# Optimization experiments

Measured on AMD Instinct MI355X. Metric: run time of the kernel, lower is better.

## Reference

```python
import jax, jax.numpy as jnp
import numpy as np

BN_EPS = 1e-3


def _bn(x, gamma, beta):
    # training-mode BatchNorm1d: per-call batch statistics (biased variance)
    m = jnp.mean(x, axis=0)
    v = jnp.mean(jnp.square(x - m), axis=0)
    return gamma * (x - m) * jax.lax.rsqrt(v + BN_EPS) + beta


def setup_inputs() -> dict:
    key = jax.random.key(0)
    ks = jax.random.split(key, 8)
    N, V, Cin, Cout = 1_000_000, 100_000, 16, 64
    return {
        "feat": jax.random.normal(ks[0], (V, Cin), dtype=jnp.float32),
        "points_xyz": jax.random.normal(ks[1], (N, Cin), dtype=jnp.float32),
        "unq_inv": jax.random.randint(ks[2], (N,), 0, V),
        "W_pre": jax.random.normal(ks[3], (Cin, Cout), dtype=jnp.float32) * (1.0 / np.sqrt(Cin)),
        "b_pre": jnp.zeros((Cout,), dtype=jnp.float32),
        "gamma_pre": jnp.ones((Cout,), dtype=jnp.float32),
        "beta_pre": jnp.zeros((Cout,), dtype=jnp.float32),
        "W_pos": jax.random.normal(ks[4], (Cout, Cout), dtype=jnp.float32) * (1.0 / np.sqrt(Cout)),
        "b_pos": jnp.zeros((Cout,), dtype=jnp.float32),
        "gamma_n": jnp.ones((Cout,), dtype=jnp.float32),
        "beta_n": jnp.zeros((Cout,), dtype=jnp.float32),
    }


def reference(feat, points_xyz, unq_inv, W_pre, b_pre, gamma_pre, beta_pre,
              W_pos, b_pos, gamma_n, beta_n):
    V = feat.shape[0]
    # per-point branch: pre_mix (Linear + BN), sin/cos gating, scatter-add to voxels
    p = _bn(points_xyz @ W_pre + b_pre, gamma_pre, beta_pre)      # [N, Cout]
    pw = p @ W_pos + b_pos                                        # [N, Cout]
    feat_add_sin = jax.ops.segment_sum(p * jnp.sin(pw), unq_inv, num_segments=V)  # [V, Cout]
    feat_add_cos = jax.ops.segment_sum(p * jnp.cos(pw), unq_inv, num_segments=V)
    # per-voxel (center) branch through the SAME pre_mix / pos_weight layers
    f = _bn(feat @ W_pre + b_pre, gamma_pre, beta_pre)            # [V, Cout]
    mw = f @ W_pos + b_pos
    center_sin = f * jnp.sin(mw)
    center_cos = f * jnp.cos(mw)
    final = (feat_add_sin + center_sin) * center_sin + (feat_add_cos + center_cos) * center_cos
    return jax.nn.relu(_bn(final, gamma_n, beta_n))
```

## Files before the change

kernel.cpp:

```cpp
#include <hip/hip_runtime.h>
#include <cstdint>
#include <cstddef>

constexpr int CIN  = 16;
constexpr int COUT = 64;
constexpr int NMOM = 16 + 136;
constexpr double BN_EPS = 1e-3;

typedef float v2f __attribute__((ext_vector_type(2)));
typedef __fp16 v2h __attribute__((ext_vector_type(2)));
constexpr float INV_2PI = 0.15915494309189535f;

constexpr int P_A = 0, P_B = 64, P_C = 128, P_WC = 192, P_SZ = 192 + CIN * COUT;

constexpr int CHUNK = 512;
constexpr int MB = 256;

__device__ __forceinline__ unsigned bc_u(v2h h) { return __builtin_bit_cast(unsigned, h); }
__device__ __forceinline__ v2h bc_h(unsigned u) { return __builtin_bit_cast(v2h, u); }

__global__ __launch_bounds__(256, 2) void moments2_kernel(const float* __restrict__ xyz, int n1,
                                                       const float* __restrict__ feat, int n2,
                                                       const int* __restrict__ unq,
                                                       int* __restrict__ cnt,
                                                       float* __restrict__ partP,
                                                       float* __restrict__ partF)
{
    const int bb  = blockIdx.x;
    const bool second = (bb >= MB);
    const float* x = second ? feat : xyz;
    const int    n = second ? n2 : n1;
    float* part    = second ? partF : partP;
    const int blk  = second ? bb - MB : bb;

    float acc[NMOM];
#pragma unroll
    for (int i = 0; i < NMOM; i++) acc[i] = 0.f;

    int tid = blk * 256 + threadIdx.x;
    int stride = MB * 256;
    for (int r = tid; r < n; r += stride) {
        const float4* xp = (const float4*)(x + (size_t)r * CIN);
        float4 a0 = xp[0], a1 = xp[1], a2 = xp[2], a3 = xp[3];
        if (!second) atomicAdd(cnt + unq[r], 1);
        float v[16] = {a0.x,a0.y,a0.z,a0.w, a1.x,a1.y,a1.z,a1.w,
                       a2.x,a2.y,a2.z,a2.w, a3.x,a3.y,a3.z,a3.w};
#pragma unroll
        for (int i = 0; i < 16; i++) acc[i] += v[i];
        int c = 16;
#pragma unroll
        for (int k = 0; k < 16; k++)
#pragma unroll
            for (int l = k; l < 16; l++) { acc[c] = fmaf(v[k], v[l], acc[c]); c++; }
    }

    const int lane = threadIdx.x & 63;
    const int wid  = threadIdx.x >> 6;
    float r0 = 0.f, r1 = 0.f, r2 = 0.f;
#pragma unroll
    for (int i = 0; i < NMOM; i++) {
        float s = acc[i];
#pragma unroll
        for (int off = 1; off < 64; off <<= 1) s += __shfl_xor(s, off, 64);
        if (i < 64)       { if (lane == i)       r0 = s; }
        else if (i < 128) { if (lane == i - 64)  r1 = s; }
        else              { if (lane == i - 128) r2 = s; }
    }

    __shared__ float red[4][NMOM];
    red[wid][lane] = r0;
    red[wid][64 + lane] = r1;
    if (lane < NMOM - 128) red[wid][128 + lane] = r2;
    __syncthreads();
    int t = threadIdx.x;
    if (t < NMOM) {
        float s = red[0][t] + red[1][t] + red[2][t] + red[3][t];
        part[(size_t)blk * NMOM + t] = s;
    }
}

__global__ __launch_bounds__(256) void prep_kernel(const float* __restrict__ Wpre, const float* __restrict__ bpre,
                            const float* __restrict__ gpre, const float* __restrict__ bepre,
                            const float* __restrict__ Wpos, const float* __restrict__ bpos,
                            const float* __restrict__ partP, const float* __restrict__ partF,
                            int nrows, int Np, int Vv,
                            float* __restrict__ prepP, float* __restrict__ prepF)
{
    const int t  = threadIdx.x;
    const int br = blockIdx.x;
    const float* part = br ? partF : partP;
    const double n    = br ? (double)Vv : (double)Np;
    const double inv_n = 1.0 / n;
    float* prep       = br ? prepF : prepP;

    __shared__ float sWpre[CIN * 64];
    __shared__ float sWpos[64 * 64];
    __shared__ double mom[NMOM];
    __shared__ double sS[64], sB[64];

    for (int i = t; i < CIN * 64; i += 256) sWpre[i] = Wpre[i];
    for (int i = t; i < 64 * 64; i += 256)  sWpos[i] = Wpos[i];

    if (t < NMOM) {
        double s0 = 0, s1 = 0, s2 = 0, s3 = 0, s4 = 0, s5 = 0, s6 = 0, s7 = 0;
        int r = 0;
        for (; r + 8 <= nrows; r += 8) {
            s0 += (double)part[(size_t)(r + 0) * NMOM + t];
            s1 += (double)part[(size_t)(r + 1) * NMOM + t];
            s2 += (double)part[(size_t)(r + 2) * NMOM + t];
            s3 += (double)part[(size_t)(r + 3) * NMOM + t];
            s4 += (double)part[(size_t)(r + 4) * NMOM + t];
            s5 += (double)part[(size_t)(r + 5) * NMOM + t];
            s6 += (double)part[(size_t)(r + 6) * NMOM + t];
            s7 += (double)part[(size_t)(r + 7) * NMOM + t];
        }
        for (; r < nrows; r++) s0 += (double)part[(size_t)r * NMOM + t];
        mom[t] = ((s0 + s1) + (s2 + s3)) + ((s4 + s5) + (s6 + s7));
    }
    __syncthreads();

    if (t < 64) {
        const int k = t;
        double mu[16];
#pragma unroll
        for (int i = 0; i < 16; i++) mu[i] = mom[i] * inv_n;
        double w[16];
#pragma unroll
        for (int i = 0; i < 16; i++) w[i] = (double)sWpre[i * 64 + k];

        double mk = (double)bpre[k];
#pragma unroll
        for (int i = 0; i < 16; i++) mk += mu[i] * w[i];

        double var = 0.0;
        int c = 16;
#pragma unroll
        for (int a = 0; a < 16; a++)
#pragma unroll
            for (int l = a; l < 16; l++) {
                double cov = mom[c] * inv_n - mu[a] * mu[l]; c++;
                var += (a == l ? 1.0 : 2.0) * w[a] * w[l] * cov;
            }

        double s_k = (double)gpre[k] / sqrt(var + BN_EPS);
        double B_k = (double)bepre[k] + s_k * ((double)bpre[k] - mk);
        sS[k] = s_k; sB[k] = B_k;
    }
    __syncthreads();

    if (t < 64) {
        const int k = t;
        double c0 = (double)bpos[k], c1 = 0.0;
        for (int j = 0; j < 64; j += 2) {
            c0 += sB[j]     * (double)sWpos[j * 64 + k];
            c1 += sB[j + 1] * (double)sWpos[(j + 1) * 64 + k];
        }
        prep[P_A + k] = (float)sS[k];
        prep[P_B + k] = (float)sB[k];
        prep[P_C + k] = (float)(c0 + c1);
    }

    {
        const int k  = t & 63;
        const int i0 = t >> 6;
        for (int i = i0; i < 16; i += 4) {
            double w0 = 0.0, w1 = 0.0;
            for (int j = 0; j < 64; j += 2) {
                w0 += (double)sWpre[i * 64 + j]     * sS[j]     * (double)sWpos[j * 64 + k];
                w1 += (double)sWpre[i * 64 + j + 1] * sS[j + 1] * (double)sWpos[(j + 1) * 64 + k];
            }
            prep[P_WC + i * 64 + k] = (float)(w0 + w1);
        }
    }
}

__global__ __launch_bounds__(256) void scan_a(const int* __restrict__ cnt, int V,
                                              int* __restrict__ chunkSum)
{
    const int b = blockIdx.x, t = threadIdx.x;
    int base = b * CHUNK;
    int i0 = base + t * 2, i1 = i0 + 1;
    int s = ((i0 < V) ? cnt[i0] : 0) + ((i1 < V) ? cnt[i1] : 0);
    __shared__ int red[4];
    const int lane = t & 63, wid = t >> 6;
#pragma unroll
    for (int off = 1; off < 64; off <<= 1) s += __shfl_xor(s, off, 64);
    if (lane == 0) red[wid] = s;
    __syncthreads();
    if (t == 0) chunkSum[b] = red[0] + red[1] + red[2] + red[3];
}

__global__ __launch_bounds__(256) void scan_b(const int* __restrict__ chunkSum, int nch,
                                              int* __restrict__ chunkBase,
                                              int* __restrict__ start, int V, int N)
{
    const int t = threadIdx.x;
    __shared__ int a[256];
    int v = (t < nch) ? chunkSum[t] : 0;
    a[t] = v;
    __syncthreads();
    for (int off = 1; off < 256; off <<= 1) {
        int add = (t >= off) ? a[t - off] : 0;
        __syncthreads();
        a[t] += add;
        __syncthreads();
    }
    chunkBase[t] = a[t] - v;
    if (t == 0) start[V] = N;
}

__global__ __launch_bounds__(64) void scan_c(const int* __restrict__ cnt, int V,
                                             const int* __restrict__ chunkBase,
                                             int* __restrict__ start)
{
    const int b = blockIdx.x;
    const int lane = threadIdx.x;
    const int base = b * CHUNK + lane * 8;
    int e[8];
    int run = 0;
#pragma unroll
    for (int j = 0; j < 8; j++) {
        int idx = base + j;
        int c = (idx < V) ? cnt[idx] : 0;
        e[j] = run;
        run += c;
    }
    int incl = run;
#pragma unroll
    for (int off = 1; off < 64; off <<= 1) {
        int vv = __shfl_up(incl, off, 64);
        if (lane >= off) incl += vv;
    }
    int excl = incl - run;
    int myBase = chunkBase[b] + excl;
#pragma unroll
    for (int j = 0; j < 8; j++) {
        int idx = base + j;
        if (idx < V) start[idx] = myBase + e[j];
    }
}

__global__ __launch_bounds__(256) void scatter_kernel(const int* __restrict__ unq, int N,
                                                      const int* __restrict__ start,
                                                      int* __restrict__ cursor,
                                                      int* __restrict__ sortedIdx)
{
    int t = blockIdx.x * blockDim.x + threadIdx.x;
    int stride = gridDim.x * blockDim.x;
    for (; t < N; t += stride) {
        int v = unq[t];
        int pos = start[v] + atomicAdd(cursor + v, 1);
        sortedIdx[pos] = t;
    }
}

__global__ __launch_bounds__(256) void fused_pass(const float* __restrict__ xyz,
                                                  const float* __restrict__ feat,
                                                  const int* __restrict__ sortedIdx,
                                                  const int* __restrict__ start,
                                                  const float* __restrict__ Wpre,
                                                  const float* __restrict__ prepP,
                                                  const float* __restrict__ prepF,
                                                  float* __restrict__ outFinal,
                                                  float* __restrict__ statsPart, int V)
{
    const int lane = threadIdx.x & 63;
    const int wid  = threadIdx.x >> 6;
    const int rq   = lane >> 2;
    const int cc   = lane & 3;

    __shared__ uint2 ldsq[4][3][64];
    __shared__ unsigned sWcF2[8 * 64];
    uint2* bufA = ldsq[wid][0];
    uint2* bufB = ldsq[wid][1];
    uint2* remb = ldsq[wid][2];
    const int wslot = rq * 4 + cc;

    for (int i = threadIdx.x; i < 8 * 64; i += 256) {
        int fi = i >> 6, ch = i & 63;
        sWcF2[i] = bc_u(__builtin_amdgcn_cvt_pkrtz(prepF[P_WC + (2 * fi) * 64 + ch],
                                                   prepF[P_WC + (2 * fi + 1) * 64 + ch]));
    }
    __syncthreads();

    v2h wpre2[8], wcp2[8];
#pragma unroll
    for (int i = 0; i < 8; i++) {
        wpre2[i] = __builtin_amdgcn_cvt_pkrtz(Wpre[(2 * i) * 64 + lane],
                                              Wpre[(2 * i + 1) * 64 + lane]);
        wcp2[i]  = __builtin_amdgcn_cvt_pkrtz(prepP[P_WC + (2 * i) * 64 + lane],
                                              prepP[P_WC + (2 * i + 1) * 64 + lane]);
    }

    const float AP = prepP[P_A + lane], BP = prepP[P_B + lane];
    const float CPr = prepP[P_C + lane] * INV_2PI;
    const float AF = prepF[P_A + lane], BF = prepF[P_B + lane];
    const float CFr = prepF[P_C + lane] * INV_2PI;

    const int wave = __builtin_amdgcn_readfirstlane((int)((blockIdx.x * blockDim.x + threadIdx.x) >> 6));
    const int nw   = (gridDim.x * blockDim.x) >> 6;
    float s1 = 0.f, s2 = 0.f;

    auto prefetch = [&](int v, int& sb, int& m, uint2& u) {
        sb = __builtin_amdgcn_readfirstlane(start[v]);
        int se = __builtin_amdgcn_readfirstlane(start[v + 1]);
        m = se - sb;
        int ms0 = min(m, 15);
        int row = min(rq, ms0);
        int ridx = sortedIdx[sb + row];
        const float* bp = (row == ms0) ? (feat + (size_t)v * CIN)
                                       : (xyz  + (size_t)ridx * CIN);
        float4 q = *(const float4*)(bp + cc * 4);
        u.x = bc_u(__builtin_amdgcn_cvt_pkrtz(q.x, q.y));
        u.y = bc_u(__builtin_amdgcn_cvt_pkrtz(q.z, q.w));
    };

    auto pointmath = [&](const uint2* buf, int j, v2f& acc) {
        uint4 a = ((const uint4*)buf)[j * 2 + 0];
        uint4 b = ((const uint4*)buf)[j * 2 + 1];
        v2h xs[8] = {bc_h(a.x), bc_h(a.y), bc_h(a.z), bc_h(a.w),
                     bc_h(b.x), bc_h(b.y), bc_h(b.z), bc_h(b.w)};
        float dx = 0.f, dw = 0.f;
#pragma unroll
        for (int i = 0; i < 8; i++) {
            dx = __builtin_amdgcn_fdot2(xs[i], wpre2[i], dx, false);
            dw = __builtin_amdgcn_fdot2(xs[i], wcp2[i],  dw, false);
        }
        float p  = fmaf(AP, dx, BP);
        float r  = fmaf(dw, INV_2PI, CPr);
        float sv = __builtin_amdgcn_sinf(r);
        float cv = __builtin_amdgcn_cosf(r);
        acc += p * (v2f){sv, cv};
    };

    int v = wave;
    int sb = 0, m = 0;
    uint2* cur = bufA;
    uint2* nxt = bufB;
    if (v < V) {
        uint2 u; prefetch(v, sb, m, u);
        cur[wslot] = u;
    }

    while (v < V) {
        const int vn = v + nw;
        int sbn = 0, mn = 0; uint2 un = {};
        if (vn < V) prefetch(vn, sbn, mn, un);

        const int ms0 = min(m, 15);
        v2f acc = (v2f){0.f, 0.f};

        for (int j = 0; j < ms0; j++) pointmath(cur, j, acc);

        for (int base = 15; base < m; base += 16) {
            const int msr  = min(16, m - base);
            const int rowc = min(rq, msr - 1);
            int ridx = sortedIdx[sb + base + rowc];
            float4 q = *(const float4*)(xyz + (size_t)ridx * CIN + cc * 4);
            uint2 u;
            u.x = bc_u(__builtin_amdgcn_cvt_pkrtz(q.x, q.y));
            u.y = bc_u(__builtin_amdgcn_cvt_pkrtz(q.z, q.w));
            remb[wslot] = u;
            for (int j = 0; j < msr; j++) pointmath(remb, j, acc);
        }

        {
            uint4 a = ((const uint4*)cur)[ms0 * 2 + 0];
            uint4 b = ((const uint4*)cur)[ms0 * 2 + 1];
            v2h xs[8] = {bc_h(a.x), bc_h(a.y), bc_h(a.z), bc_h(a.w),
                         bc_h(b.x), bc_h(b.y), bc_h(b.z), bc_h(b.w)};
            float dx = 0.f, dw = 0.f;
#pragma unroll
            for (int i = 0; i < 8; i++) {
                dx = __builtin_amdgcn_fdot2(xs[i], wpre2[i], dx, false);
                dw = __builtin_amdgcn_fdot2(xs[i], bc_h(sWcF2[i * 64 + lane]), dw, false);
            }
            float f  = fmaf(AF, dx, BF);
            float r  = fmaf(dw, INV_2PI, CFr);
            float sv = __builtin_amdgcn_sinf(r);
            float cv = __builtin_amdgcn_cosf(r);
            float cs = f * sv, ccn = f * cv;
            float fin = fmaf(acc.x + cs, cs, (acc.y + ccn) * ccn);
            outFinal[(size_t)v * 64 + lane] = fin;
            s1 += fin;
            s2 = fmaf(fin, fin, s2);
        }

        if (vn < V) nxt[wslot] = un;
        uint2* tmp = cur; cur = nxt; nxt = tmp;
        v = vn; sb = sbn; m = mn;
    }

    __shared__ float sh1[4][64], sh2[4][64];
    sh1[wid][lane] = s1; sh2[wid][lane] = s2;
    __syncthreads();
    if (threadIdx.x < 64) {
        float t1 = sh1[0][lane] + sh1[1][lane] + sh1[2][lane] + sh1[3][lane];
        float t2 = sh2[0][lane] + sh2[1][lane] + sh2[2][lane] + sh2[3][lane];
        float* row = statsPart + (size_t)(blockIdx.x & 63) * 128;
        atomicAdd(row + lane, t1);
        atomicAdd(row + 64 + lane, t2);
    }
}

__global__ __launch_bounds__(256) void norm_kernel(float* __restrict__ out,
                                                   const float* __restrict__ sp,
                                                   const float* __restrict__ gn,
                                                   const float* __restrict__ bnb,
                                                   int V, size_t n4)
{
    __shared__ float sNs[64], sNb[64];
    const int t = threadIdx.x;
    if (t < 64) {
        double u1 = 0.0, u2 = 0.0;
#pragma unroll 4
        for (int r = 0; r < 64; r++) {
            u1 += (double)sp[(size_t)r * 128 + t];
            u2 += (double)sp[(size_t)r * 128 + 64 + t];
        }
        double mean = u1 / (double)V;
        double var  = u2 / (double)V - mean * mean;
        double ns   = (double)gn[t] / sqrt(var + BN_EPS);
        sNs[t] = (float)ns;
        sNb[t] = (float)((double)bnb[t] - ns * mean);
    }
    __syncthreads();

    const float4* ns4 = (const float4*)sNs;
    const float4* nb4 = (const float4*)sNb;
    float4* o4 = (float4*)out;
    size_t i = (size_t)blockIdx.x * blockDim.x + threadIdx.x;
    size_t stride = (size_t)gridDim.x * blockDim.x;
    for (; i < n4; i += stride) {
        int g = (int)(i & 15);
        float4 sc = ns4[g], bi = nb4[g];
        float4 w = o4[i];
        w.x = fmaxf(0.f, fmaf(sc.x, w.x, bi.x));
        w.y = fmaxf(0.f, fmaf(sc.y, w.y, bi.y));
        w.z = fmaxf(0.f, fmaf(sc.z, w.z, bi.z));
        w.w = fmaxf(0.f, fmaf(sc.w, w.w, bi.w));
        o4[i] = w;
    }
}

extern "C" void kernel_launch(void* const* d_in, const int* in_sizes, int n_in,
                              void* d_out, int out_size, void* d_ws, size_t ws_size,
                              hipStream_t stream)
{
    const float* feat  = (const float*)d_in[0];
    const float* xyz   = (const float*)d_in[1];
    const int*   unq   = (const int*)d_in[2];
    const float* Wpre  = (const float*)d_in[3];
    const float* bpre  = (const float*)d_in[4];
    const float* gpre  = (const float*)d_in[5];
    const float* bepre = (const float*)d_in[6];
    const float* Wpos  = (const float*)d_in[7];
    const float* bpos  = (const float*)d_in[8];
    const float* gn    = (const float*)d_in[9];
    const float* bnb   = (const float*)d_in[10];

    const int V = in_sizes[0] / CIN;
    const int N = in_sizes[1] / CIN;
    const int nch = (V + CHUNK - 1) / CHUNK;

    char* ws = (char*)d_ws;
    size_t off = 0;
    auto alloc = [&](size_t bytes) { void* p = ws + off; off += (bytes + 255) & ~size_t(255); return p; };

    int*   cnt       = (int*)alloc((size_t)V * 4);
    int*   cursor    = (int*)alloc((size_t)V * 4);
    float* statsPart = (float*)alloc(64 * 128 * 4);
    const size_t zeroBytes = off;

    int*   start     = (int*)alloc((size_t)(V + 1) * 4);
    int*   chunkSum  = (int*)alloc(256 * 4);
    int*   chunkBase = (int*)alloc(256 * 4);
    int*   sortedIdx = (int*)alloc((size_t)(N + 64) * 4);

    float* partP = (float*)alloc((size_t)MB * NMOM * 4);
    float* partF = (float*)alloc((size_t)MB * NMOM * 4);
    float* prepP = (float*)alloc(P_SZ * 4);
    float* prepF = (float*)alloc(P_SZ * 4);

    hipMemsetAsync(d_ws, 0, zeroBytes, stream);

    moments2_kernel<<<2 * MB, 256, 0, stream>>>(xyz, N, feat, V, unq, cnt, partP, partF);
    scan_a<<<nch, 256, 0, stream>>>(cnt, V, chunkSum);
    scan_b<<<1, 256, 0, stream>>>(chunkSum, nch, chunkBase, start, V, N);
    scan_c<<<nch, 64, 0, stream>>>(cnt, V, chunkBase, start);
    scatter_kernel<<<1024, 256, 0, stream>>>(unq, N, start, cursor, sortedIdx);
    prep_kernel<<<2, 256, 0, stream>>>(Wpre, bpre, gpre, bepre, Wpos, bpos,
                                       partP, partF, MB, N, V, prepP, prepF);
    fused_pass<<<2048, 256, 0, stream>>>(xyz, feat, sortedIdx, start, Wpre,
                                         prepP, prepF, (float*)d_out, statsPart, V);
    norm_kernel<<<512, 256, 0, stream>>>((float*)d_out, statsPart, gn, bnb, V,
                                         (size_t)out_size / 4);
}
```

Measured before the change: 225.3 us.

## Merge prep with scan_a, fold scan_b into scanC, zero cursor in scan

The BN-parameter prep kernel now runs in the same launch as the per-chunk count reduction, as two extra blocks. The single-block chunk-prefix kernel is dropped: each scanC block sums the preceding chunk totals itself with a wave reduction. scanC also zeroes the cursor array, so the memset covers fewer bytes. The aim is to cut two kernel launches and their serialization gaps, at the cost of redundant prefix reads in scanC (up to about 196 chunk sums per block) and a prep launch whose two heavy blocks share it with many light ones.

```diff
diff --git a/kernel.cpp b/kernel.cpp
--- a/kernel.cpp
+++ b/kernel.cpp
@@ -79,14 +79,32 @@
     }
 }
 
-__global__ __launch_bounds__(256) void prep_kernel(const float* __restrict__ Wpre, const float* __restrict__ bpre,
+__global__ __launch_bounds__(256) void prep_scanA(const float* __restrict__ Wpre, const float* __restrict__ bpre,
                             const float* __restrict__ gpre, const float* __restrict__ bepre,
                             const float* __restrict__ Wpos, const float* __restrict__ bpos,
                             const float* __restrict__ partP, const float* __restrict__ partF,
                             int nrows, int Np, int Vv,
-                            float* __restrict__ prepP, float* __restrict__ prepF)
-{
-    const int t  = threadIdx.x;
+                            float* __restrict__ prepP, float* __restrict__ prepF,
+                            const int* __restrict__ cnt, int V,
+                            int* __restrict__ chunkSum)
+{
+    const int t = threadIdx.x;
+    const int lane = t & 63, wid = t >> 6;
+
+    if (blockIdx.x >= 2) {
+        const int b = blockIdx.x - 2;
+        int base = b * CHUNK;
+        int i0 = base + t * 2, i1 = i0 + 1;
+        int s = ((i0 < V) ? cnt[i0] : 0) + ((i1 < V) ? cnt[i1] : 0);
+        __shared__ int redc[4];
+#pragma unroll
+        for (int off = 1; off < 64; off <<= 1) s += __shfl_xor(s, off, 64);
+        if (lane == 0) redc[wid] = s;
+        __syncthreads();
+        if (t == 0) chunkSum[b] = redc[0] + redc[1] + redc[2] + redc[3];
+        return;
+    }
+
     const int br = blockIdx.x;
     const float* part = br ? partF : partP;
     const double n    = br ? (double)Vv : (double)Np;
@@ -174,47 +192,20 @@
     }
 }
 
-__global__ __launch_bounds__(256) void scan_a(const int* __restrict__ cnt, int V,
-                                              int* __restrict__ chunkSum)
-{
-    const int b = blockIdx.x, t = threadIdx.x;
-    int base = b * CHUNK;
-    int i0 = base + t * 2, i1 = i0 + 1;
-    int s = ((i0 < V) ? cnt[i0] : 0) + ((i1 < V) ? cnt[i1] : 0);
-    __shared__ int red[4];
-    const int lane = t & 63, wid = t >> 6;
-#pragma unroll
-    for (int off = 1; off < 64; off <<= 1) s += __shfl_xor(s, off, 64);
-    if (lane == 0) red[wid] = s;
-    __syncthreads();
-    if (t == 0) chunkSum[b] = red[0] + red[1] + red[2] + red[3];
-}
-
-__global__ __launch_bounds__(256) void scan_b(const int* __restrict__ chunkSum, int nch,
-                                              int* __restrict__ chunkBase,
-                                              int* __restrict__ start, int V, int N)
-{
-    const int t = threadIdx.x;
-    __shared__ int a[256];
-    int v = (t < nch) ? chunkSum[t] : 0;
-    a[t] = v;
-    __syncthreads();
-    for (int off = 1; off < 256; off <<= 1) {
-        int add = (t >= off) ? a[t - off] : 0;
-        __syncthreads();
-        a[t] += add;
-        __syncthreads();
-    }
-    chunkBase[t] = a[t] - v;
-    if (t == 0) start[V] = N;
-}
-
-__global__ __launch_bounds__(64) void scan_c(const int* __restrict__ cnt, int V,
-                                             const int* __restrict__ chunkBase,
-                                             int* __restrict__ start)
+__global__ __launch_bounds__(64) void scanC(const int* __restrict__ cnt, int V, int N,
+                                            const int* __restrict__ chunkSum,
+                                            int* __restrict__ start,
+                                            int* __restrict__ cursor)
 {
     const int b = blockIdx.x;
     const int lane = threadIdx.x;
+
+    int pv = 0;
+    for (int i = lane; i < b; i += 64) pv += chunkSum[i];
+#pragma unroll
+    for (int off = 1; off < 64; off <<= 1) pv += __shfl_xor(pv, off, 64);
+    const int chunkBase = pv;
+
     const int base = b * CHUNK + lane * 8;
     int e[8];
     int run = 0;
@@ -232,12 +223,13 @@
         if (lane >= off) incl += vv;
     }
     int excl = incl - run;
-    int myBase = chunkBase[b] + excl;
+    int myBase = chunkBase + excl;
 #pragma unroll
     for (int j = 0; j < 8; j++) {
         int idx = base + j;
-        if (idx < V) start[idx] = myBase + e[j];
-    }
+        if (idx < V) { start[idx] = myBase + e[j]; cursor[idx] = 0; }
+    }
+    if (b == 0 && lane == 0) start[V] = N;
 }
 
 __global__ __launch_bounds__(256) void scatter_kernel(const int* __restrict__ unq, int N,
@@ -468,13 +460,12 @@
     auto alloc = [&](size_t bytes) { void* p = ws + off; off += (bytes + 255) & ~size_t(255); return p; };
 
     int*   cnt       = (int*)alloc((size_t)V * 4);
-    int*   cursor    = (int*)alloc((size_t)V * 4);
     float* statsPart = (float*)alloc(64 * 128 * 4);
     const size_t zeroBytes = off;
 
+    int*   cursor    = (int*)alloc((size_t)V * 4);
     int*   start     = (int*)alloc((size_t)(V + 1) * 4);
     int*   chunkSum  = (int*)alloc(256 * 4);
-    int*   chunkBase = (int*)alloc(256 * 4);
     int*   sortedIdx = (int*)alloc((size_t)(N + 64) * 4);
 
     float* partP = (float*)alloc((size_t)MB * NMOM * 4);
@@ -485,12 +476,11 @@
     hipMemsetAsync(d_ws, 0, zeroBytes, stream);
 
     moments2_kernel<<<2 * MB, 256, 0, stream>>>(xyz, N, feat, V, unq, cnt, partP, partF);
-    scan_a<<<nch, 256, 0, stream>>>(cnt, V, chunkSum);
-    scan_b<<<1, 256, 0, stream>>>(chunkSum, nch, chunkBase, start, V, N);
-    scan_c<<<nch, 64, 0, stream>>>(cnt, V, chunkBase, start);
+    prep_scanA<<<nch + 2, 256, 0, stream>>>(Wpre, bpre, gpre, bepre, Wpos, bpos,
+                                            partP, partF, MB, N, V, prepP, prepF,
+                                            cnt, V, chunkSum);
+    scanC<<<nch, 64, 0, stream>>>(cnt, V, N, chunkSum, start, cursor);
     scatter_kernel<<<1024, 256, 0, stream>>>(unq, N, start, cursor, sortedIdx);
-    prep_kernel<<<2, 256, 0, stream>>>(Wpre, bpre, gpre, bepre, Wpos, bpos,
-                                       partP, partF, MB, N, V, prepP, prepF);
     fused_pass<<<2048, 256, 0, stream>>>(xyz, feat, sortedIdx, start, Wpre,
                                          prepP, prepF, (float*)d_out, statsPart, V);
     norm_kernel<<<512, 256, 0, stream>>>((float*)d_out, statsPart, gn, bnb, V,
```

New measurement: 222.3 us. About the same (-1.3%).
